# Optimization experiments

Measured on AMD Instinct MI355X. Metric: run time of the kernel, lower is better.

The kernel has to match this reference:

```python
import jax, jax.numpy as jnp
import numpy as np

MAX_NUM_CENTERS = 100
CENTER_IGNORE_PX = 3
SIGMA = 2.0   # center_gt_blur
KSIZE = 21    # GaussianLayer kernel size (ReflectionPad2d(10) + Conv2d(k=21))


def _gauss_kernel():
    r = KSIZE // 2
    x = jnp.arange(-r, r + 1, dtype=jnp.float32)
    g = jnp.exp(-0.5 * (x / SIGMA) ** 2)
    g = g / g.sum()
    return jnp.outer(g, g)  # [21,21], sums to 1 (matches scipy gaussian_filter of a delta)


def _gaussian_blur(x):
    # x: [B,H,W] -> depthwise 21x21 gaussian with reflect padding (GaussianLayer)
    r = KSIZE // 2
    k = _gauss_kernel()[None, None]  # [1,1,21,21]
    xp = jnp.pad(x[:, None], ((0, 0), (0, 0), (r, r), (r, r)), mode="reflect")
    y = jax.lax.conv_general_dilated(xp, k, (1, 1), "VALID",
                                     dimension_numbers=("NCHW", "OIHW", "NCHW"))
    return y[:, 0]


def setup_inputs() -> dict:
    key = jax.random.key(0)
    k1, k2 = jax.random.split(key)
    B, H, W = 8, 768, 768
    instances = jax.random.randint(k1, (B, 1, H, W), 0, MAX_NUM_CENTERS, dtype=jnp.int32)
    centers = jax.random.uniform(k2, (B, MAX_NUM_CENTERS, 2), dtype=jnp.float32) * (H - 1) + 1.0
    return {"instances": instances, "centers": centers}


def reference(instances, centers):
    B, _, H, W = instances.shape
    inst = instances[:, 0]                                # [B,H,W]
    col = jnp.arange(W, dtype=jnp.float32)                # xym_s[0][i,j] = j
    row = jnp.arange(H, dtype=jnp.float32)[:, None]       # xym_s[1][i,j] = i

    valid = inst > 0                                      # instance_mask
    has_inst = jnp.any(valid, axis=(1, 2)).astype(jnp.float32)  # len(unique)>1 gate

    # per-pixel nearest-center gather: center = centers[b, id-1]
    idx = jnp.clip(inst - 1, 0, MAX_NUM_CENTERS - 1)
    c = centers[jnp.arange(B)[:, None, None], idx]        # [B,H,W,2]
    gt_cx = jnp.where(valid, c[..., 1], -10000.0)         # gt_center_x (swapped coords)
    gt_cy = jnp.where(valid, c[..., 0], -10000.0)

    gt_X = gt_cx - row                                    # gt_center_x - xym_s[1]
    gt_Y = gt_cy - col                                    # gt_center_y - xym_s[0]

    near = (jnp.abs(gt_X) < CENTER_IGNORE_PX) & (jnp.abs(gt_Y) < CENTER_IGNORE_PX)
    # batches with no instances skip the block -> ignore stays all-ones
    ignore = jnp.where(has_inst[:, None, None] > 0, (~near).astype(jnp.float32), 1.0)

    m = valid.astype(jnp.float32)
    R = jnp.sqrt(gt_X ** 2 + gt_Y ** 2) * m
    theta_raw = jnp.arctan2(gt_Y, gt_X)
    theta = theta_raw * has_inst[:, None, None]           # skipped (zero) when no instances
    s = jnp.sin(theta_raw) * m
    cth = jnp.cos(theta_raw) * m
    M = jnp.sqrt(s ** 2 + cth ** 2)                       # == m, kept for faithfulness
    s = jnp.where(valid, s / jnp.maximum(M, 1e-12), 0.0)
    cth = jnp.where(valid, cth / jnp.maximum(M, 1e-12), 0.0)

    # gt_center_mask: zeros if no center-neighborhood pixels, else normalized blur
    blur = _gaussian_blur(1.0 - ignore)
    all_ones = jnp.all(ignore >= 1.0, axis=(1, 2))        # gt_center_mask.all()
    bmax = jnp.max(blur, axis=(1, 2), keepdims=True)
    cmask = jnp.where(all_ones[:, None, None], 0.0, blur / jnp.maximum(bmax, 1e-12))

    top = jnp.stack([R, theta, s, cth, ignore, cmask], axis=1)       # [B,6,H,W]
    mat = jnp.concatenate([top, jnp.zeros((B, 7, H, W), top.dtype)], axis=1)[:, :, None]
    # mat: [B,13,1,H,W]; channels 6..12 are zero (no orientation input)

    # gt_centers[id] = centers[b, id-1][[1,0]] for each instance id present
    present = jnp.zeros((B, MAX_NUM_CENTERS), dtype=bool).at[
        jnp.arange(B)[:, None], inst.reshape(B, -1)].set(True)
    swapped = centers[..., ::-1]
    gt_centers = jnp.zeros_like(centers).at[:, 1:, :].set(
        jnp.where(present[:, 1:, None], swapped[:, :-1, :], 0.0))

    return mat, gt_centers
```

## Files before the change

### kernel.cpp

```cpp
#include <hip/hip_runtime.h>
#include <math.h>

#define NB 8
#define NH 768
#define NW 768
#define NHW (NH*NW)
#define NCEN 100
#define NPIX (NB*NHW)
#define RAD 10
#define KS 21

#define SCAN_BLKS (NPIX / 4096)
#define BLKS_PER_B (NHW / 4096)
#define CAND_BLKS 96
#define ZBLKS 1344
#define ZPB 6144
#define ZBLK_PER_B 168
#define MID_BLKS (NB*CAND_BLKS + ZBLKS)
#define NPQ 3
#define FBLK_PX (NPQ*1024)
#define QBLK3_PER_B (NHW / FBLK_PX)
#define BSLOT 24
#define BCAP 23
#define GCAP 256
#define FCAP 256

#define STORE(v, p) (*(p) = (v))

#define OFF_MASKS 0
#define OFF_BLIST 4608
#define OFF_BMAXP 32256
#define OFF_HAS   33024
#define OFF_M     33032
#define OFF_GLIST 33040
#define WS_INTS   35088

typedef float f4 __attribute__((ext_vector_type(4)));

__device__ const float g_G[KS] = {
    7.4335e-7f, 7.9919e-6f, 6.6915e-5f, 0.00043634f, 0.00221592f,
    0.00876415f, 0.02699548f, 0.06475880f, 0.12098536f, 0.17603266f,
    0.19947114f,
    0.17603266f, 0.12098536f, 0.06475880f, 0.02699548f, 0.00876415f,
    0.00221592f, 0.00043634f, 6.6915e-5f, 7.9919e-6f, 7.4335e-7f};

__device__ __forceinline__ float wfun(int p, int q, const float* __restrict__ g) {
    int d = p - q;
    float w = 0.f;
    if (d >= -RAD && d <= RAD) w = g[d + RAD];
    int a = p + q;
    if (q > 0 && a <= RAD) w += g[a + RAD];
    if (q < NH - 1 && a >= 2 * (NH - 1) - RAD) w += g[a - 2 * (NH - 1) + RAD];
    return w;
}

__device__ __forceinline__ float fatan2(float Y, float X) {
    float ax = fabsf(X), ay = fabsf(Y);
    float mx = fmaxf(ax, ay), mn = fminf(ax, ay);
    float a = mx > 0.f ? __fdividef(mn, mx) : 0.f;
    float ss = a * a;
    float r = fmaf(fmaf(fmaf(fmaf(fmaf(-0.01172120f, ss, 0.05265332f), ss,
                -0.11643287f), ss, 0.19354346f), ss, -0.33262347f), ss, 0.99997726f) * a;
    if (ay > ax) r = 1.57079637f - r;
    if (X < 0.f) r = 3.14159274f - r;
    return copysignf(r, Y);
}

template <bool U8>
__global__ __launch_bounds__(256) void k_scan(const int4* __restrict__ inst4,
                                              const float* __restrict__ centers,
                                              int* __restrict__ ws,
                                              unsigned char* __restrict__ u8) {
    __shared__ unsigned sm[4];
    __shared__ float2 s_c2[NCEN];
    __shared__ int s_loc[BCAP];
    __shared__ int s_lcnt;
    __shared__ unsigned s_u8[1024];
    int t = threadIdx.x;
    int blk = blockIdx.x;
    int b = blk / BLKS_PER_B;
    int lblk = blk - b * BLKS_PER_B;
    if (t < 4) sm[t] = 0;
    if (t == 0) s_lcnt = 0;
    for (int k = t; k < NCEN; k += 256)
        s_c2[k] = ((const float2*)centers)[b * NCEN + k];
    __syncthreads();

    unsigned m0 = 0, m1 = 0, m2 = 0, m3 = 0;
    size_t base = (size_t)blk * 1024 + t;
    int ppb = lblk * 4096 + t * 4;
#pragma unroll
    for (int q = 0; q < 4; q++) {
        int4 v = inst4[base + (size_t)q * 256];
        int pp = ppb + q * 1024;
        int i = pp / NW;
        int j0 = pp - i * NW;
        if (U8) {
            unsigned packed = ((unsigned)v.x & 255u) | (((unsigned)v.y & 255u) << 8) |
                              (((unsigned)v.z & 255u) << 16) | (((unsigned)v.w & 255u) << 24);
            s_u8[q * 256 + t] = packed;
        }
        int a[4] = {v.x, v.y, v.z, v.w};
#pragma unroll
        for (int e = 0; e < 4; e++) {
            int iv = a[e];
            if (iv > 0) {
                unsigned bit = 1u << (iv & 31);
                int w = iv >> 5;
                if (w == 0) m0 |= bit; else if (w == 1) m1 |= bit;
                else if (w == 2) m2 |= bit; else m3 |= bit;
                int idx = iv - 1;
                idx = idx > NCEN - 1 ? NCEN - 1 : idx;
                float2 c = s_c2[idx];
                if (fabsf(c.y - (float)i) < 3.f && fabsf(c.x - (float)(j0 + e)) < 3.f) {
                    int slot = atomicAdd(&s_lcnt, 1);
                    if (slot < BCAP) s_loc[slot] = (i << 16) | (j0 + e);
                }
            }
        }
    }
#pragma unroll
    for (int off = 32; off >= 1; off >>= 1) {
        m0 |= __shfl_xor(m0, off);
        m1 |= __shfl_xor(m1, off);
        m2 |= __shfl_xor(m2, off);
        m3 |= __shfl_xor(m3, off);
    }
    if ((t & 63) == 0) {
        if (m0) atomicOr(&sm[0], m0);
        if (m1) atomicOr(&sm[1], m1);
        if (m2) atomicOr(&sm[2], m2);
        if (m3) atomicOr(&sm[3], m3);
    }
    __syncthreads();
    if (U8) {
        int4 vv = ((const int4*)s_u8)[t];
        *(int4*)&u8[(size_t)blk * 4096 + t * 16] = vv;
    }
    if (t < 4) ws[OFF_MASKS + blk * 4 + t] = (int)sm[t];
    int cnt = s_lcnt < BCAP ? s_lcnt : BCAP;
    int* slot = &ws[OFF_BLIST + blk * BSLOT];
    if (t == 0) slot[0] = cnt;
    if (t < cnt) slot[1 + t] = s_loc[t];
}

__global__ __launch_bounds__(256) void k_mid(const float* __restrict__ centers,
                                             int* __restrict__ ws,
                                             float* __restrict__ out) {
    int t = threadIdx.x;
    int g = blockIdx.x;

    if (g < NB * CAND_BLKS) {
        __shared__ float s_g[KS];
        __shared__ int s_list[GCAP];
        __shared__ int s_tot;
        __shared__ unsigned s_m[4];
        __shared__ float s_red[4];
        int b = g / CAND_BLKS;
        int cb = g - b * CAND_BLKS;
        if (t < KS) s_g[t] = g_G[t];
        if (t == 0) s_tot = 0;
        if (t < 4) s_m[t] = 0;
        __syncthreads();
        if (t < BLKS_PER_B) {
            const int* slot = &ws[OFF_BLIST + (b * BLKS_PER_B + t) * BSLOT];
            int cnt = slot[0];
            cnt = cnt < 0 ? 0 : (cnt > BCAP ? BCAP : cnt);
            int basep = atomicAdd(&s_tot, cnt);
            for (int i2 = 0; i2 < cnt; i2++) {
                int s = basep + i2;
                if (s < GCAP) s_list[s] = slot[1 + i2];
            }
            if (cb == 0) {
                const unsigned* pm = (const unsigned*)&ws[OFF_MASKS + (b * BLKS_PER_B + t) * 4];
                unsigned w0 = pm[0], w1 = pm[1], w2 = pm[2], w3 = pm[3];
                if (w0) atomicOr(&s_m[0], w0);
                if (w1) atomicOr(&s_m[1], w1);
                if (w2) atomicOr(&s_m[2], w2);
                if (w3) atomicOr(&s_m[3], w3);
            }
        }
        __syncthreads();
        int M = s_tot < GCAP ? s_tot : GCAP;

        if (cb == 0) {
            float* gt = out + (size_t)NB * 13 * NHW;
            if (t < NCEN) {
                float vx = 0.f, vy = 0.f;
                if (t >= 1 && ((s_m[t >> 5] >> (t & 31)) & 1u)) {
                    vx = centers[(b * NCEN + (t - 1)) * 2 + 1];
                    vy = centers[(b * NCEN + (t - 1)) * 2 + 0];
                }
                gt[(b * NCEN + t) * 2 + 0] = vx;
                gt[(b * NCEN + t) * 2 + 1] = vy;
            }
            if (t == 0) {
                unsigned any = (s_m[0] & 0xFFFFFFFEu) | s_m[1] | s_m[2] | s_m[3];
                ws[OFF_HAS + b] = any ? 1 : 0;
                ws[OFF_M + b] = M;
            }
            for (int e = t; e < M; e += 256) ws[OFF_GLIST + b * GCAP + e] = s_list[e];
        }

        float lmax = 0.f;
        int total = M * (KS * KS);
        for (int c = cb * 256 + t; c < total; c += CAND_BLKS * 256) {
            int m = c / (KS * KS), r = c - m * (KS * KS);
            int e = s_list[m];
            int pi = (e >> 16) + r / KS - RAD;
            int pj = (e & 0xFFFF) + (r - (r / KS) * KS) - RAD;
            if (pi < 0 || pi >= NH || pj < 0 || pj >= NW) continue;
            float acc = 0.f;
            for (int m2 = 0; m2 < M; m2++) {
                int e2 = s_list[m2];
                float wi = wfun(pi, e2 >> 16, s_g);
                if (wi == 0.f) continue;
                acc += wi * wfun(pj, e2 & 0xFFFF, s_g);
            }
            lmax = fmaxf(lmax, acc);
        }
#pragma unroll
        for (int off = 32; off >= 1; off >>= 1) lmax = fmaxf(lmax, __shfl_down(lmax, off));
        if ((t & 63) == 0) s_red[t >> 6] = lmax;
        __syncthreads();
        if (t == 0) {
            float bmx = fmaxf(fmaxf(s_red[0], s_red[1]), fmaxf(s_red[2], s_red[3]));
            ((float*)ws)[OFF_BMAXP + b * CAND_BLKS + cb] = bmx;
        }
    } else {
        int zblk = g - NB * CAND_BLKS;
        int b2 = zblk / ZBLK_PER_B;
        int rem0 = (zblk - b2 * ZBLK_PER_B) * ZPB;
        f4 z = {0.f, 0.f, 0.f, 0.f};
        f4* dst = (f4*)out + (size_t)b2 * (13 * NHW / 4) + (6 * NHW / 4) + rem0 + t;
#pragma unroll
        for (int it = 0; it < ZPB / 256; ++it)
            STORE(z, dst + it * 256);
    }
}

template <bool U8>
__global__ __launch_bounds__(256) void k_fused(const int* __restrict__ inst,
                                               const unsigned char* __restrict__ u8,
                                               const float* __restrict__ centers,
                                               const int* __restrict__ ws,
                                               float* __restrict__ out) {
    __shared__ float s_cen[2 * NCEN];
    __shared__ float s_g[KS];
    __shared__ int s_fl[FCAP];
    __shared__ int s_fM;
    __shared__ unsigned s_bm;
    int t = threadIdx.x;
    int b = blockIdx.x / QBLK3_PER_B;
    int qblk = blockIdx.x - b * QBLK3_PER_B;

    int has = ws[OFF_HAS + b];
    int M = ws[OFF_M + b];
    for (int k = t; k < 2 * NCEN; k += 256) s_cen[k] = centers[b * 2 * NCEN + k];
    if (t < KS) s_g[t] = g_G[t];
    if (t == 255) s_fM = 0;
    if (t == 254) s_bm = 0;
    __syncthreads();

    if (t < CAND_BLKS)
        atomicMax(&s_bm, __float_as_uint(((const float*)ws)[OFF_BMAXP + b * CAND_BLKS + t]));

    int p0blk = qblk * FBLK_PX;
    int r0 = qblk * 4;
    const int* gl = &ws[OFF_GLIST + b * GCAP];
    for (int m = t; m < M; m += 256) {
        int e = gl[m];
        int qi = e >> 16;
        bool keep = false;
#pragma unroll
        for (int rr = 0; rr < 4; rr++) keep |= (wfun(r0 + rr, qi, s_g) != 0.f);
        if (keep) {
            int slot = atomicAdd(&s_fM, 1);
            if (slot < FCAP) s_fl[slot] = e;
        }
    }
    __syncthreads();
    int FM = s_fM < FCAP ? s_fM : FCAP;
    float bmx = __uint_as_float(s_bm);
    float sc = (has && M > 0) ? 1.f / fmaxf(bmx, 1e-12f) : 0.f;

    float* outb = out + (size_t)b * 13 * NHW;

    for (int qq = 0; qq < NPQ; ++qq) {
        int p0 = p0blk + qq * 1024 + t * 4;
        int gi = p0 / NW;
        int gj0 = p0 - gi * NW;

        int ia[4];
        if (U8) {
            unsigned v8 = *(const unsigned*)&u8[(size_t)b * NHW + p0];
            ia[0] = v8 & 255; ia[1] = (v8 >> 8) & 255; ia[2] = (v8 >> 16) & 255; ia[3] = v8 >> 24;
        } else {
            int4 ivv = *(const int4*)&inst[(size_t)b * NHW + p0];
            ia[0] = ivv.x; ia[1] = ivv.y; ia[2] = ivv.z; ia[3] = ivv.w;
        }
        f4 vR, vTh, vS, vC, vIg;
#pragma unroll
        for (int e = 0; e < 4; e++) {
            int iv = ia[e];
            bool valid = iv > 0;
            int idx = iv - 1;
            idx = idx < 0 ? 0 : idx;
            float cy = s_cen[2 * idx];
            float cx = s_cen[2 * idx + 1];
            float gcx = valid ? cx : -10000.f;
            float gcy = valid ? cy : -10000.f;
            float X = gcx - (float)gi;
            float Y = gcy - (float)(gj0 + e);
            bool near = (fabsf(X) < 3.f) && (fabsf(Y) < 3.f);
            vIg[e] = (has != 0) ? (near ? 0.f : 1.f) : 1.f;
            float m = valid ? 1.f : 0.f;
            float R2 = X * X + Y * Y;
            vR[e] = sqrtf(R2) * m;
            float rinv = R2 > 0.f ? rsqrtf(R2) : 0.f;
            vS[e] = valid ? Y * rinv : 0.f;
            vC[e] = valid ? (R2 > 0.f ? X * rinv : 1.f) : 0.f;
            float th = fatan2(Y, X);
            vTh[e] = (has != 0) ? th : 0.f;
        }

        f4 blur = {0.f, 0.f, 0.f, 0.f};
        for (int m = 0; m < FM; m++) {
            int e2 = s_fl[m];
            float wi = wfun(gi, e2 >> 16, s_g);
            if (wi == 0.f) continue;
            int qj = e2 & 0xFFFF;
#pragma unroll
            for (int e = 0; e < 4; e++) blur[e] += wi * wfun(gj0 + e, qj, s_g);
        }
        f4 vCm = blur * sc;

        STORE(vR,  (f4*)&outb[(size_t)0 * NHW + p0]);
        STORE(vTh, (f4*)&outb[(size_t)1 * NHW + p0]);
        STORE(vS,  (f4*)&outb[(size_t)2 * NHW + p0]);
        STORE(vC,  (f4*)&outb[(size_t)3 * NHW + p0]);
        STORE(vIg, (f4*)&outb[(size_t)4 * NHW + p0]);
        STORE(vCm, (f4*)&outb[(size_t)5 * NHW + p0]);
    }
}

extern "C" void kernel_launch(void* const* d_in, const int* in_sizes, int n_in,
                              void* d_out, int out_size, void* d_ws, size_t ws_size,
                              hipStream_t stream) {
    const int* inst = (const int*)d_in[0];
    const float* centers = (const float*)d_in[1];
    float* out = (float*)d_out;
    int* ws = (int*)d_ws;
    unsigned char* u8 = (unsigned char*)d_ws + (size_t)WS_INTS * 4;
    bool use_u8 = ws_size >= (size_t)WS_INTS * 4 + (size_t)NPIX;

    if (use_u8) {
        k_scan<true><<<SCAN_BLKS, 256, 0, stream>>>((const int4*)inst, centers, ws, u8);
        k_mid<<<MID_BLKS, 256, 0, stream>>>(centers, ws, out);
        k_fused<true><<<NB * QBLK3_PER_B, 256, 0, stream>>>(inst, u8, centers, ws, out);
    } else {
        k_scan<false><<<SCAN_BLKS, 256, 0, stream>>>((const int4*)inst, centers, ws, u8);
        k_mid<<<MID_BLKS, 256, 0, stream>>>(centers, ws, out);
        k_fused<false><<<NB * QBLK3_PER_B, 256, 0, stream>>>(inst, u8, centers, ws, out);
    }
}
```

Measured before the change: 271.9 us.

## Compute per-pixel geometry channels and zero fill in the scan kernel

```diff
diff --git a/kernel.cpp b/kernel.cpp
--- a/kernel.cpp
+++ b/kernel.cpp
@@ -13,10 +13,6 @@
 #define SCAN_BLKS (NPIX / 4096)
 #define BLKS_PER_B (NHW / 4096)
 #define CAND_BLKS 96
-#define ZBLKS 1344
-#define ZPB 6144
-#define ZBLK_PER_B 168
-#define MID_BLKS (NB*CAND_BLKS + ZBLKS)
 #define NPQ 3
 #define FBLK_PX (NPQ*1024)
 #define QBLK3_PER_B (NHW / FBLK_PX)
@@ -33,7 +29,6 @@
 #define OFF_HAS   33024
 #define OFF_M     33032
 #define OFF_GLIST 33040
-#define WS_INTS   35088
 
 typedef float f4 __attribute__((ext_vector_type(4)));
 
@@ -66,16 +61,14 @@
     return copysignf(r, Y);
 }
 
-template <bool U8>
-__global__ __launch_bounds__(256) void k_scan(const int4* __restrict__ inst4,
+__global__ __launch_bounds__(256) void k_main(const int4* __restrict__ inst4,
                                               const float* __restrict__ centers,
                                               int* __restrict__ ws,
-                                              unsigned char* __restrict__ u8) {
+                                              float* __restrict__ out) {
     __shared__ unsigned sm[4];
     __shared__ float2 s_c2[NCEN];
     __shared__ int s_loc[BCAP];
     __shared__ int s_lcnt;
-    __shared__ unsigned s_u8[1024];
     int t = threadIdx.x;
     int blk = blockIdx.x;
     int b = blk / BLKS_PER_B;
@@ -89,35 +82,55 @@
     unsigned m0 = 0, m1 = 0, m2 = 0, m3 = 0;
     size_t base = (size_t)blk * 1024 + t;
     int ppb = lblk * 4096 + t * 4;
+    float* outb = out + (size_t)b * 13 * NHW;
+    const f4 z = {0.f, 0.f, 0.f, 0.f};
 #pragma unroll
     for (int q = 0; q < 4; q++) {
         int4 v = inst4[base + (size_t)q * 256];
         int pp = ppb + q * 1024;
-        int i = pp / NW;
-        int j0 = pp - i * NW;
-        if (U8) {
-            unsigned packed = ((unsigned)v.x & 255u) | (((unsigned)v.y & 255u) << 8) |
-                              (((unsigned)v.z & 255u) << 16) | (((unsigned)v.w & 255u) << 24);
-            s_u8[q * 256 + t] = packed;
-        }
-        int a[4] = {v.x, v.y, v.z, v.w};
+        int gi = pp / NW;
+        int gj0 = pp - gi * NW;
+        int ia[4] = {v.x, v.y, v.z, v.w};
+        f4 vR, vTh, vS, vC, vIg;
 #pragma unroll
         for (int e = 0; e < 4; e++) {
-            int iv = a[e];
-            if (iv > 0) {
+            int iv = ia[e];
+            bool valid = iv > 0;
+            if (valid) {
                 unsigned bit = 1u << (iv & 31);
                 int w = iv >> 5;
                 if (w == 0) m0 |= bit; else if (w == 1) m1 |= bit;
                 else if (w == 2) m2 |= bit; else m3 |= bit;
-                int idx = iv - 1;
-                idx = idx > NCEN - 1 ? NCEN - 1 : idx;
-                float2 c = s_c2[idx];
-                if (fabsf(c.y - (float)i) < 3.f && fabsf(c.x - (float)(j0 + e)) < 3.f) {
-                    int slot = atomicAdd(&s_lcnt, 1);
-                    if (slot < BCAP) s_loc[slot] = (i << 16) | (j0 + e);
-                }
             }
-        }
+            int idx = iv - 1;
+            idx = idx < 0 ? 0 : (idx > NCEN - 1 ? NCEN - 1 : idx);
+            float2 c = s_c2[idx];
+            float gcx = valid ? c.y : -10000.f;
+            float gcy = valid ? c.x : -10000.f;
+            float X = gcx - (float)gi;
+            float Y = gcy - (float)(gj0 + e);
+            bool near = (fabsf(X) < 3.f) && (fabsf(Y) < 3.f);
+            if (valid && near) {
+                int slot = atomicAdd(&s_lcnt, 1);
+                if (slot < BCAP) s_loc[slot] = (gi << 16) | (gj0 + e);
+            }
+            vIg[e] = near ? 0.f : 1.f;
+            float m = valid ? 1.f : 0.f;
+            float R2 = X * X + Y * Y;
+            vR[e] = sqrtf(R2) * m;
+            float rinv = R2 > 0.f ? rsqrtf(R2) : 0.f;
+            vS[e] = valid ? Y * rinv : 0.f;
+            vC[e] = valid ? (R2 > 0.f ? X * rinv : 1.f) : 0.f;
+            vTh[e] = fatan2(Y, X);
+        }
+        STORE(vR,  (f4*)&outb[(size_t)0 * NHW + pp]);
+        STORE(vTh, (f4*)&outb[(size_t)1 * NHW + pp]);
+        STORE(vS,  (f4*)&outb[(size_t)2 * NHW + pp]);
+        STORE(vC,  (f4*)&outb[(size_t)3 * NHW + pp]);
+        STORE(vIg, (f4*)&outb[(size_t)4 * NHW + pp]);
+#pragma unroll
+        for (int ch = 6; ch < 13; ++ch)
+            STORE(z, (f4*)&outb[(size_t)ch * NHW + pp]);
     }
 #pragma unroll
     for (int off = 32; off >= 1; off >>= 1) {
@@ -133,10 +146,6 @@
         if (m3) atomicOr(&sm[3], m3);
     }
     __syncthreads();
-    if (U8) {
-        int4 vv = ((const int4*)s_u8)[t];
-        *(int4*)&u8[(size_t)blk * 4096 + t * 16] = vv;
-    }
     if (t < 4) ws[OFF_MASKS + blk * 4 + t] = (int)sm[t];
     int cnt = s_lcnt < BCAP ? s_lcnt : BCAP;
     int* slot = &ws[OFF_BLIST + blk * BSLOT];
@@ -144,108 +153,90 @@
     if (t < cnt) slot[1 + t] = s_loc[t];
 }
 
-__global__ __launch_bounds__(256) void k_mid(const float* __restrict__ centers,
-                                             int* __restrict__ ws,
-                                             float* __restrict__ out) {
+__global__ __launch_bounds__(256) void k_bmax(const float* __restrict__ centers,
+                                              int* __restrict__ ws,
+                                              float* __restrict__ out) {
+    __shared__ float s_g[KS];
+    __shared__ int s_list[GCAP];
+    __shared__ int s_tot;
+    __shared__ unsigned s_m[4];
+    __shared__ float s_red[4];
     int t = threadIdx.x;
-    int g = blockIdx.x;
-
-    if (g < NB * CAND_BLKS) {
-        __shared__ float s_g[KS];
-        __shared__ int s_list[GCAP];
-        __shared__ int s_tot;
-        __shared__ unsigned s_m[4];
-        __shared__ float s_red[4];
-        int b = g / CAND_BLKS;
-        int cb = g - b * CAND_BLKS;
-        if (t < KS) s_g[t] = g_G[t];
-        if (t == 0) s_tot = 0;
-        if (t < 4) s_m[t] = 0;
-        __syncthreads();
-        if (t < BLKS_PER_B) {
-            const int* slot = &ws[OFF_BLIST + (b * BLKS_PER_B + t) * BSLOT];
-            int cnt = slot[0];
-            cnt = cnt < 0 ? 0 : (cnt > BCAP ? BCAP : cnt);
-            int basep = atomicAdd(&s_tot, cnt);
-            for (int i2 = 0; i2 < cnt; i2++) {
-                int s = basep + i2;
-                if (s < GCAP) s_list[s] = slot[1 + i2];
+    int b = blockIdx.x / CAND_BLKS;
+    int cb = blockIdx.x - b * CAND_BLKS;
+    if (t < KS) s_g[t] = g_G[t];
+    if (t == 0) s_tot = 0;
+    if (t < 4) s_m[t] = 0;
+    __syncthreads();
+    if (t < BLKS_PER_B) {
+        const int* slot = &ws[OFF_BLIST + (b * BLKS_PER_B + t) * BSLOT];
+        int cnt = slot[0];
+        cnt = cnt < 0 ? 0 : (cnt > BCAP ? BCAP : cnt);
+        int basep = atomicAdd(&s_tot, cnt);
+        for (int i2 = 0; i2 < cnt; i2++) {
+            int s = basep + i2;
+            if (s < GCAP) s_list[s] = slot[1 + i2];
+        }
+        if (cb == 0) {
+            const unsigned* pm = (const unsigned*)&ws[OFF_MASKS + (b * BLKS_PER_B + t) * 4];
+            unsigned w0 = pm[0], w1 = pm[1], w2 = pm[2], w3 = pm[3];
+            if (w0) atomicOr(&s_m[0], w0);
+            if (w1) atomicOr(&s_m[1], w1);
+            if (w2) atomicOr(&s_m[2], w2);
+            if (w3) atomicOr(&s_m[3], w3);
+        }
+    }
+    __syncthreads();
+    int M = s_tot < GCAP ? s_tot : GCAP;
+
+    if (cb == 0) {
+        float* gt = out + (size_t)NB * 13 * NHW;
+        if (t < NCEN) {
+            float vx = 0.f, vy = 0.f;
+            if (t >= 1 && ((s_m[t >> 5] >> (t & 31)) & 1u)) {
+                vx = centers[(b * NCEN + (t - 1)) * 2 + 1];
+                vy = centers[(b * NCEN + (t - 1)) * 2 + 0];
             }
-            if (cb == 0) {
-                const unsigned* pm = (const unsigned*)&ws[OFF_MASKS + (b * BLKS_PER_B + t) * 4];
-                unsigned w0 = pm[0], w1 = pm[1], w2 = pm[2], w3 = pm[3];
-                if (w0) atomicOr(&s_m[0], w0);
-                if (w1) atomicOr(&s_m[1], w1);
-                if (w2) atomicOr(&s_m[2], w2);
-                if (w3) atomicOr(&s_m[3], w3);
-            }
-        }
-        __syncthreads();
-        int M = s_tot < GCAP ? s_tot : GCAP;
-
-        if (cb == 0) {
-            float* gt = out + (size_t)NB * 13 * NHW;
-            if (t < NCEN) {
-                float vx = 0.f, vy = 0.f;
-                if (t >= 1 && ((s_m[t >> 5] >> (t & 31)) & 1u)) {
-                    vx = centers[(b * NCEN + (t - 1)) * 2 + 1];
-                    vy = centers[(b * NCEN + (t - 1)) * 2 + 0];
-                }
-                gt[(b * NCEN + t) * 2 + 0] = vx;
-                gt[(b * NCEN + t) * 2 + 1] = vy;
-            }
-            if (t == 0) {
-                unsigned any = (s_m[0] & 0xFFFFFFFEu) | s_m[1] | s_m[2] | s_m[3];
-                ws[OFF_HAS + b] = any ? 1 : 0;
-                ws[OFF_M + b] = M;
-            }
-            for (int e = t; e < M; e += 256) ws[OFF_GLIST + b * GCAP + e] = s_list[e];
-        }
-
-        float lmax = 0.f;
-        int total = M * (KS * KS);
-        for (int c = cb * 256 + t; c < total; c += CAND_BLKS * 256) {
-            int m = c / (KS * KS), r = c - m * (KS * KS);
-            int e = s_list[m];
-            int pi = (e >> 16) + r / KS - RAD;
-            int pj = (e & 0xFFFF) + (r - (r / KS) * KS) - RAD;
-            if (pi < 0 || pi >= NH || pj < 0 || pj >= NW) continue;
-            float acc = 0.f;
-            for (int m2 = 0; m2 < M; m2++) {
-                int e2 = s_list[m2];
-                float wi = wfun(pi, e2 >> 16, s_g);
-                if (wi == 0.f) continue;
-                acc += wi * wfun(pj, e2 & 0xFFFF, s_g);
-            }
-            lmax = fmaxf(lmax, acc);
-        }
-#pragma unroll
-        for (int off = 32; off >= 1; off >>= 1) lmax = fmaxf(lmax, __shfl_down(lmax, off));
-        if ((t & 63) == 0) s_red[t >> 6] = lmax;
-        __syncthreads();
+            gt[(b * NCEN + t) * 2 + 0] = vx;
+            gt[(b * NCEN + t) * 2 + 1] = vy;
+        }
         if (t == 0) {
-            float bmx = fmaxf(fmaxf(s_red[0], s_red[1]), fmaxf(s_red[2], s_red[3]));
-            ((float*)ws)[OFF_BMAXP + b * CAND_BLKS + cb] = bmx;
-        }
-    } else {
-        int zblk = g - NB * CAND_BLKS;
-        int b2 = zblk / ZBLK_PER_B;
-        int rem0 = (zblk - b2 * ZBLK_PER_B) * ZPB;
-        f4 z = {0.f, 0.f, 0.f, 0.f};
-        f4* dst = (f4*)out + (size_t)b2 * (13 * NHW / 4) + (6 * NHW / 4) + rem0 + t;
-#pragma unroll
-        for (int it = 0; it < ZPB / 256; ++it)
-            STORE(z, dst + it * 256);
-    }
-}
-
-template <bool U8>
-__global__ __launch_bounds__(256) void k_fused(const int* __restrict__ inst,
-                                               const unsigned char* __restrict__ u8,
-                                               const float* __restrict__ centers,
-                                               const int* __restrict__ ws,
+            unsigned any = (s_m[0] & 0xFFFFFFFEu) | s_m[1] | s_m[2] | s_m[3];
+            ws[OFF_HAS + b] = any ? 1 : 0;
+            ws[OFF_M + b] = M;
+        }
+        for (int e = t; e < M; e += 256) ws[OFF_GLIST + b * GCAP + e] = s_list[e];
+    }
+
+    float lmax = 0.f;
+    int total = M * (KS * KS);
+    for (int c = cb * 256 + t; c < total; c += CAND_BLKS * 256) {
+        int m = c / (KS * KS), r = c - m * (KS * KS);
+        int e = s_list[m];
+        int pi = (e >> 16) + r / KS - RAD;
+        int pj = (e & 0xFFFF) + (r - (r / KS) * KS) - RAD;
+        if (pi < 0 || pi >= NH || pj < 0 || pj >= NW) continue;
+        float acc = 0.f;
+        for (int m2 = 0; m2 < M; m2++) {
+            int e2 = s_list[m2];
+            float wi = wfun(pi, e2 >> 16, s_g);
+            if (wi == 0.f) continue;
+            acc += wi * wfun(pj, e2 & 0xFFFF, s_g);
+        }
+        lmax = fmaxf(lmax, acc);
+    }
+#pragma unroll
+    for (int off = 32; off >= 1; off >>= 1) lmax = fmaxf(lmax, __shfl_down(lmax, off));
+    if ((t & 63) == 0) s_red[t >> 6] = lmax;
+    __syncthreads();
+    if (t == 0) {
+        float bmx = fmaxf(fmaxf(s_red[0], s_red[1]), fmaxf(s_red[2], s_red[3]));
+        ((float*)ws)[OFF_BMAXP + b * CAND_BLKS + cb] = bmx;
+    }
+}
+
+__global__ __launch_bounds__(256) void k_cmask(const int* __restrict__ ws,
                                                float* __restrict__ out) {
-    __shared__ float s_cen[2 * NCEN];
     __shared__ float s_g[KS];
     __shared__ int s_fl[FCAP];
     __shared__ int s_fM;
@@ -256,7 +247,6 @@
 
     int has = ws[OFF_HAS + b];
     int M = ws[OFF_M + b];
-    for (int k = t; k < 2 * NCEN; k += 256) s_cen[k] = centers[b * 2 * NCEN + k];
     if (t < KS) s_g[t] = g_G[t];
     if (t == 255) s_fM = 0;
     if (t == 254) s_bm = 0;
@@ -285,45 +275,11 @@
     float sc = (has && M > 0) ? 1.f / fmaxf(bmx, 1e-12f) : 0.f;
 
     float* outb = out + (size_t)b * 13 * NHW;
-
+    const f4 z = {0.f, 0.f, 0.f, 0.f};
     for (int qq = 0; qq < NPQ; ++qq) {
         int p0 = p0blk + qq * 1024 + t * 4;
         int gi = p0 / NW;
         int gj0 = p0 - gi * NW;
-
-        int ia[4];
-        if (U8) {
-            unsigned v8 = *(const unsigned*)&u8[(size_t)b * NHW + p0];
-            ia[0] = v8 & 255; ia[1] = (v8 >> 8) & 255; ia[2] = (v8 >> 16) & 255; ia[3] = v8 >> 24;
-        } else {
-            int4 ivv = *(const int4*)&inst[(size_t)b * NHW + p0];
-            ia[0] = ivv.x; ia[1] = ivv.y; ia[2] = ivv.z; ia[3] = ivv.w;
-        }
-        f4 vR, vTh, vS, vC, vIg;
-#pragma unroll
-        for (int e = 0; e < 4; e++) {
-            int iv = ia[e];
-            bool valid = iv > 0;
-            int idx = iv - 1;
-            idx = idx < 0 ? 0 : idx;
-            float cy = s_cen[2 * idx];
-            float cx = s_cen[2 * idx + 1];
-            float gcx = valid ? cx : -10000.f;
-            float gcy = valid ? cy : -10000.f;
-            float X = gcx - (float)gi;
-            float Y = gcy - (float)(gj0 + e);
-            bool near = (fabsf(X) < 3.f) && (fabsf(Y) < 3.f);
-            vIg[e] = (has != 0) ? (near ? 0.f : 1.f) : 1.f;
-            float m = valid ? 1.f : 0.f;
-            float R2 = X * X + Y * Y;
-            vR[e] = sqrtf(R2) * m;
-            float rinv = R2 > 0.f ? rsqrtf(R2) : 0.f;
-            vS[e] = valid ? Y * rinv : 0.f;
-            vC[e] = valid ? (R2 > 0.f ? X * rinv : 1.f) : 0.f;
-            float th = fatan2(Y, X);
-            vTh[e] = (has != 0) ? th : 0.f;
-        }
-
         f4 blur = {0.f, 0.f, 0.f, 0.f};
         for (int m = 0; m < FM; m++) {
             int e2 = s_fl[m];
@@ -334,13 +290,9 @@
             for (int e = 0; e < 4; e++) blur[e] += wi * wfun(gj0 + e, qj, s_g);
         }
         f4 vCm = blur * sc;
-
-        STORE(vR,  (f4*)&outb[(size_t)0 * NHW + p0]);
-        STORE(vTh, (f4*)&outb[(size_t)1 * NHW + p0]);
-        STORE(vS,  (f4*)&outb[(size_t)2 * NHW + p0]);
-        STORE(vC,  (f4*)&outb[(size_t)3 * NHW + p0]);
-        STORE(vIg, (f4*)&outb[(size_t)4 * NHW + p0]);
         STORE(vCm, (f4*)&outb[(size_t)5 * NHW + p0]);
+        if (!has)
+            STORE(z, (f4*)&outb[(size_t)1 * NHW + p0]);
     }
 }
 
@@ -351,16 +303,8 @@
     const float* centers = (const float*)d_in[1];
     float* out = (float*)d_out;
     int* ws = (int*)d_ws;
-    unsigned char* u8 = (unsigned char*)d_ws + (size_t)WS_INTS * 4;
-    bool use_u8 = ws_size >= (size_t)WS_INTS * 4 + (size_t)NPIX;
-
-    if (use_u8) {
-        k_scan<true><<<SCAN_BLKS, 256, 0, stream>>>((const int4*)inst, centers, ws, u8);
-        k_mid<<<MID_BLKS, 256, 0, stream>>>(centers, ws, out);
-        k_fused<true><<<NB * QBLK3_PER_B, 256, 0, stream>>>(inst, u8, centers, ws, out);
-    } else {
-        k_scan<false><<<SCAN_BLKS, 256, 0, stream>>>((const int4*)inst, centers, ws, u8);
-        k_mid<<<MID_BLKS, 256, 0, stream>>>(centers, ws, out);
-        k_fused<false><<<NB * QBLK3_PER_B, 256, 0, stream>>>(inst, u8, centers, ws, out);
-    }
-}
+
+    k_main<<<SCAN_BLKS, 256, 0, stream>>>((const int4*)inst, centers, ws, out);
+    k_bmax<<<NB * CAND_BLKS, 256, 0, stream>>>(centers, ws, out);
+    k_cmask<<<NB * QBLK3_PER_B, 256, 0, stream>>>(ws, out);
+}
```

After: 294.7 us. 8.4% more time.

## Split output work per channel plane and move zero-fill into the output kernel

Applied to the files above, without the earlier changes.

```diff
diff --git a/kernel.cpp b/kernel.cpp
--- a/kernel.cpp
+++ b/kernel.cpp
@@ -13,17 +13,13 @@
 #define SCAN_BLKS (NPIX / 4096)
 #define BLKS_PER_B (NHW / 4096)
 #define CAND_BLKS 96
-#define ZBLKS 1344
-#define ZPB 6144
-#define ZBLK_PER_B 168
-#define MID_BLKS (NB*CAND_BLKS + ZBLKS)
-#define NPQ 3
-#define FBLK_PX (NPQ*1024)
-#define QBLK3_PER_B (NHW / FBLK_PX)
+#define CHUNKS 24
+#define CHUNK_F4 6144
+#define OUT_BLKS (NB*13*CHUNKS)
 #define BSLOT 24
 #define BCAP 23
 #define GCAP 256
-#define FCAP 256
+#define FCAP 96
 
 #define STORE(v, p) (*(p) = (v))
 
@@ -144,203 +140,202 @@
     if (t < cnt) slot[1 + t] = s_loc[t];
 }
 
-__global__ __launch_bounds__(256) void k_mid(const float* __restrict__ centers,
-                                             int* __restrict__ ws,
+__global__ __launch_bounds__(256) void k_bmax(const float* __restrict__ centers,
+                                              int* __restrict__ ws,
+                                              float* __restrict__ out) {
+    __shared__ float s_g[KS];
+    __shared__ int s_list[GCAP];
+    __shared__ int s_tot;
+    __shared__ unsigned s_m[4];
+    __shared__ float s_red[4];
+    int t = threadIdx.x;
+    int b = blockIdx.x / CAND_BLKS;
+    int cb = blockIdx.x - b * CAND_BLKS;
+    if (t < KS) s_g[t] = g_G[t];
+    if (t == 0) s_tot = 0;
+    if (t < 4) s_m[t] = 0;
+    __syncthreads();
+    if (t < BLKS_PER_B) {
+        const int* slot = &ws[OFF_BLIST + (b * BLKS_PER_B + t) * BSLOT];
+        int cnt = slot[0];
+        cnt = cnt < 0 ? 0 : (cnt > BCAP ? BCAP : cnt);
+        int basep = atomicAdd(&s_tot, cnt);
+        for (int i2 = 0; i2 < cnt; i2++) {
+            int s = basep + i2;
+            if (s < GCAP) s_list[s] = slot[1 + i2];
+        }
+        if (cb == 0) {
+            const unsigned* pm = (const unsigned*)&ws[OFF_MASKS + (b * BLKS_PER_B + t) * 4];
+            unsigned w0 = pm[0], w1 = pm[1], w2 = pm[2], w3 = pm[3];
+            if (w0) atomicOr(&s_m[0], w0);
+            if (w1) atomicOr(&s_m[1], w1);
+            if (w2) atomicOr(&s_m[2], w2);
+            if (w3) atomicOr(&s_m[3], w3);
+        }
+    }
+    __syncthreads();
+    int M = s_tot < GCAP ? s_tot : GCAP;
+
+    if (cb == 0) {
+        float* gt = out + (size_t)NB * 13 * NHW;
+        if (t < NCEN) {
+            float vx = 0.f, vy = 0.f;
+            if (t >= 1 && ((s_m[t >> 5] >> (t & 31)) & 1u)) {
+                vx = centers[(b * NCEN + (t - 1)) * 2 + 1];
+                vy = centers[(b * NCEN + (t - 1)) * 2 + 0];
+            }
+            gt[(b * NCEN + t) * 2 + 0] = vx;
+            gt[(b * NCEN + t) * 2 + 1] = vy;
+        }
+        if (t == 0) {
+            unsigned any = (s_m[0] & 0xFFFFFFFEu) | s_m[1] | s_m[2] | s_m[3];
+            ws[OFF_HAS + b] = any ? 1 : 0;
+            ws[OFF_M + b] = M;
+        }
+        for (int e = t; e < M; e += 256) ws[OFF_GLIST + b * GCAP + e] = s_list[e];
+    }
+
+    float lmax = 0.f;
+    int total = M * (KS * KS);
+    for (int c = cb * 256 + t; c < total; c += CAND_BLKS * 256) {
+        int m = c / (KS * KS), r = c - m * (KS * KS);
+        int e = s_list[m];
+        int pi = (e >> 16) + r / KS - RAD;
+        int pj = (e & 0xFFFF) + (r - (r / KS) * KS) - RAD;
+        if (pi < 0 || pi >= NH || pj < 0 || pj >= NW) continue;
+        float acc = 0.f;
+        for (int m2 = 0; m2 < M; m2++) {
+            int e2 = s_list[m2];
+            float wi = wfun(pi, e2 >> 16, s_g);
+            if (wi == 0.f) continue;
+            acc += wi * wfun(pj, e2 & 0xFFFF, s_g);
+        }
+        lmax = fmaxf(lmax, acc);
+    }
+#pragma unroll
+    for (int off = 32; off >= 1; off >>= 1) lmax = fmaxf(lmax, __shfl_down(lmax, off));
+    if ((t & 63) == 0) s_red[t >> 6] = lmax;
+    __syncthreads();
+    if (t == 0) {
+        float bmx = fmaxf(fmaxf(s_red[0], s_red[1]), fmaxf(s_red[2], s_red[3]));
+        ((float*)ws)[OFF_BMAXP + b * CAND_BLKS + cb] = bmx;
+    }
+}
+
+template <bool U8>
+__global__ __launch_bounds__(256) void k_out(const int* __restrict__ inst,
+                                             const unsigned char* __restrict__ u8,
+                                             const float* __restrict__ centers,
+                                             const int* __restrict__ ws,
                                              float* __restrict__ out) {
     int t = threadIdx.x;
-    int g = blockIdx.x;
-
-    if (g < NB * CAND_BLKS) {
+    int blk = blockIdx.x;
+    int plane = blk / CHUNKS;
+    int chunk = blk - plane * CHUNKS;
+    int b = plane / 13;
+    int ch = plane - b * 13;
+    f4* dst = (f4*)(out + (size_t)b * 13 * NHW + (size_t)ch * NHW) + chunk * CHUNK_F4;
+
+    if (ch >= 6) {
+        const f4 z = {0.f, 0.f, 0.f, 0.f};
+#pragma unroll
+        for (int it = 0; it < CHUNK_F4 / 256; ++it) STORE(z, dst + it * 256 + t);
+        return;
+    }
+
+    if (ch == 5) {
         __shared__ float s_g[KS];
-        __shared__ int s_list[GCAP];
-        __shared__ int s_tot;
-        __shared__ unsigned s_m[4];
-        __shared__ float s_red[4];
-        int b = g / CAND_BLKS;
-        int cb = g - b * CAND_BLKS;
+        __shared__ int s_fl[FCAP];
+        __shared__ int s_fM;
+        __shared__ unsigned s_bm;
+        int has = ws[OFF_HAS + b];
+        int M = ws[OFF_M + b];
         if (t < KS) s_g[t] = g_G[t];
-        if (t == 0) s_tot = 0;
-        if (t < 4) s_m[t] = 0;
+        if (t == 255) s_fM = 0;
+        if (t == 254) s_bm = 0;
         __syncthreads();
-        if (t < BLKS_PER_B) {
-            const int* slot = &ws[OFF_BLIST + (b * BLKS_PER_B + t) * BSLOT];
-            int cnt = slot[0];
-            cnt = cnt < 0 ? 0 : (cnt > BCAP ? BCAP : cnt);
-            int basep = atomicAdd(&s_tot, cnt);
-            for (int i2 = 0; i2 < cnt; i2++) {
-                int s = basep + i2;
-                if (s < GCAP) s_list[s] = slot[1 + i2];
-            }
-            if (cb == 0) {
-                const unsigned* pm = (const unsigned*)&ws[OFF_MASKS + (b * BLKS_PER_B + t) * 4];
-                unsigned w0 = pm[0], w1 = pm[1], w2 = pm[2], w3 = pm[3];
-                if (w0) atomicOr(&s_m[0], w0);
-                if (w1) atomicOr(&s_m[1], w1);
-                if (w2) atomicOr(&s_m[2], w2);
-                if (w3) atomicOr(&s_m[3], w3);
+        if (t < CAND_BLKS)
+            atomicMax(&s_bm, __float_as_uint(((const float*)ws)[OFF_BMAXP + b * CAND_BLKS + t]));
+        int r0 = chunk * 32;
+        const int* gl = &ws[OFF_GLIST + b * GCAP];
+        for (int m = t; m < M; m += 256) {
+            int e = gl[m];
+            int qi = e >> 16;
+            if (qi >= r0 - RAD && qi < r0 + 32 + RAD) {
+                int slot = atomicAdd(&s_fM, 1);
+                if (slot < FCAP) s_fl[slot] = e;
             }
         }
         __syncthreads();
-        int M = s_tot < GCAP ? s_tot : GCAP;
-
-        if (cb == 0) {
-            float* gt = out + (size_t)NB * 13 * NHW;
-            if (t < NCEN) {
-                float vx = 0.f, vy = 0.f;
-                if (t >= 1 && ((s_m[t >> 5] >> (t & 31)) & 1u)) {
-                    vx = centers[(b * NCEN + (t - 1)) * 2 + 1];
-                    vy = centers[(b * NCEN + (t - 1)) * 2 + 0];
-                }
-                gt[(b * NCEN + t) * 2 + 0] = vx;
-                gt[(b * NCEN + t) * 2 + 1] = vy;
-            }
-            if (t == 0) {
-                unsigned any = (s_m[0] & 0xFFFFFFFEu) | s_m[1] | s_m[2] | s_m[3];
-                ws[OFF_HAS + b] = any ? 1 : 0;
-                ws[OFF_M + b] = M;
-            }
-            for (int e = t; e < M; e += 256) ws[OFF_GLIST + b * GCAP + e] = s_list[e];
-        }
-
-        float lmax = 0.f;
-        int total = M * (KS * KS);
-        for (int c = cb * 256 + t; c < total; c += CAND_BLKS * 256) {
-            int m = c / (KS * KS), r = c - m * (KS * KS);
-            int e = s_list[m];
-            int pi = (e >> 16) + r / KS - RAD;
-            int pj = (e & 0xFFFF) + (r - (r / KS) * KS) - RAD;
-            if (pi < 0 || pi >= NH || pj < 0 || pj >= NW) continue;
-            float acc = 0.f;
-            for (int m2 = 0; m2 < M; m2++) {
-                int e2 = s_list[m2];
-                float wi = wfun(pi, e2 >> 16, s_g);
+        int FM = s_fM < FCAP ? s_fM : FCAP;
+        float sc = (has && M > 0) ? 1.f / fmaxf(__uint_as_float(s_bm), 1e-12f) : 0.f;
+        for (int it = 0; it < CHUNK_F4 / 256; ++it) {
+            int f = chunk * CHUNK_F4 + it * 256 + t;
+            int p0 = f * 4;
+            int gi = p0 / NW, gj0 = p0 - gi * NW;
+            f4 blur = {0.f, 0.f, 0.f, 0.f};
+            for (int m = 0; m < FM; m++) {
+                int e2 = s_fl[m];
+                float wi = wfun(gi, e2 >> 16, s_g);
                 if (wi == 0.f) continue;
-                acc += wi * wfun(pj, e2 & 0xFFFF, s_g);
-            }
-            lmax = fmaxf(lmax, acc);
-        }
-#pragma unroll
-        for (int off = 32; off >= 1; off >>= 1) lmax = fmaxf(lmax, __shfl_down(lmax, off));
-        if ((t & 63) == 0) s_red[t >> 6] = lmax;
-        __syncthreads();
-        if (t == 0) {
-            float bmx = fmaxf(fmaxf(s_red[0], s_red[1]), fmaxf(s_red[2], s_red[3]));
-            ((float*)ws)[OFF_BMAXP + b * CAND_BLKS + cb] = bmx;
-        }
-    } else {
-        int zblk = g - NB * CAND_BLKS;
-        int b2 = zblk / ZBLK_PER_B;
-        int rem0 = (zblk - b2 * ZBLK_PER_B) * ZPB;
-        f4 z = {0.f, 0.f, 0.f, 0.f};
-        f4* dst = (f4*)out + (size_t)b2 * (13 * NHW / 4) + (6 * NHW / 4) + rem0 + t;
-#pragma unroll
-        for (int it = 0; it < ZPB / 256; ++it)
-            STORE(z, dst + it * 256);
-    }
-}
-
-template <bool U8>
-__global__ __launch_bounds__(256) void k_fused(const int* __restrict__ inst,
-                                               const unsigned char* __restrict__ u8,
-                                               const float* __restrict__ centers,
-                                               const int* __restrict__ ws,
-                                               float* __restrict__ out) {
-    __shared__ float s_cen[2 * NCEN];
-    __shared__ float s_g[KS];
-    __shared__ int s_fl[FCAP];
-    __shared__ int s_fM;
-    __shared__ unsigned s_bm;
-    int t = threadIdx.x;
-    int b = blockIdx.x / QBLK3_PER_B;
-    int qblk = blockIdx.x - b * QBLK3_PER_B;
-
+                int qj = e2 & 0xFFFF;
+#pragma unroll
+                for (int e = 0; e < 4; e++) blur[e] += wi * wfun(gj0 + e, qj, s_g);
+            }
+            f4 v = blur * sc;
+            STORE(v, dst + it * 256 + t);
+        }
+        return;
+    }
+
+    __shared__ float2 s_c2[NCEN];
+    for (int k = t; k < NCEN; k += 256)
+        s_c2[k] = ((const float2*)centers)[b * NCEN + k];
     int has = ws[OFF_HAS + b];
-    int M = ws[OFF_M + b];
-    for (int k = t; k < 2 * NCEN; k += 256) s_cen[k] = centers[b * 2 * NCEN + k];
-    if (t < KS) s_g[t] = g_G[t];
-    if (t == 255) s_fM = 0;
-    if (t == 254) s_bm = 0;
-    __syncthreads();
-
-    if (t < CAND_BLKS)
-        atomicMax(&s_bm, __float_as_uint(((const float*)ws)[OFF_BMAXP + b * CAND_BLKS + t]));
-
-    int p0blk = qblk * FBLK_PX;
-    int r0 = qblk * 4;
-    const int* gl = &ws[OFF_GLIST + b * GCAP];
-    for (int m = t; m < M; m += 256) {
-        int e = gl[m];
-        int qi = e >> 16;
-        bool keep = false;
-#pragma unroll
-        for (int rr = 0; rr < 4; rr++) keep |= (wfun(r0 + rr, qi, s_g) != 0.f);
-        if (keep) {
-            int slot = atomicAdd(&s_fM, 1);
-            if (slot < FCAP) s_fl[slot] = e;
-        }
-    }
-    __syncthreads();
-    int FM = s_fM < FCAP ? s_fM : FCAP;
-    float bmx = __uint_as_float(s_bm);
-    float sc = (has && M > 0) ? 1.f / fmaxf(bmx, 1e-12f) : 0.f;
-
-    float* outb = out + (size_t)b * 13 * NHW;
-
-    for (int qq = 0; qq < NPQ; ++qq) {
-        int p0 = p0blk + qq * 1024 + t * 4;
-        int gi = p0 / NW;
-        int gj0 = p0 - gi * NW;
-
+    __syncthreads();
+    for (int it = 0; it < CHUNK_F4 / 256; ++it) {
+        int f = chunk * CHUNK_F4 + it * 256 + t;
+        int p0 = f * 4;
+        int gi = p0 / NW, gj0 = p0 - gi * NW;
         int ia[4];
         if (U8) {
             unsigned v8 = *(const unsigned*)&u8[(size_t)b * NHW + p0];
-            ia[0] = v8 & 255; ia[1] = (v8 >> 8) & 255; ia[2] = (v8 >> 16) & 255; ia[3] = v8 >> 24;
+            ia[0] = v8 & 255; ia[1] = (v8 >> 8) & 255;
+            ia[2] = (v8 >> 16) & 255; ia[3] = v8 >> 24;
         } else {
             int4 ivv = *(const int4*)&inst[(size_t)b * NHW + p0];
             ia[0] = ivv.x; ia[1] = ivv.y; ia[2] = ivv.z; ia[3] = ivv.w;
         }
-        f4 vR, vTh, vS, vC, vIg;
+        f4 o;
 #pragma unroll
         for (int e = 0; e < 4; e++) {
             int iv = ia[e];
             bool valid = iv > 0;
             int idx = iv - 1;
             idx = idx < 0 ? 0 : idx;
-            float cy = s_cen[2 * idx];
-            float cx = s_cen[2 * idx + 1];
-            float gcx = valid ? cx : -10000.f;
-            float gcy = valid ? cy : -10000.f;
+            float2 c = s_c2[idx];
+            float gcx = valid ? c.y : -10000.f;
+            float gcy = valid ? c.x : -10000.f;
             float X = gcx - (float)gi;
             float Y = gcy - (float)(gj0 + e);
-            bool near = (fabsf(X) < 3.f) && (fabsf(Y) < 3.f);
-            vIg[e] = (has != 0) ? (near ? 0.f : 1.f) : 1.f;
-            float m = valid ? 1.f : 0.f;
-            float R2 = X * X + Y * Y;
-            vR[e] = sqrtf(R2) * m;
-            float rinv = R2 > 0.f ? rsqrtf(R2) : 0.f;
-            vS[e] = valid ? Y * rinv : 0.f;
-            vC[e] = valid ? (R2 > 0.f ? X * rinv : 1.f) : 0.f;
-            float th = fatan2(Y, X);
-            vTh[e] = (has != 0) ? th : 0.f;
-        }
-
-        f4 blur = {0.f, 0.f, 0.f, 0.f};
-        for (int m = 0; m < FM; m++) {
-            int e2 = s_fl[m];
-            float wi = wfun(gi, e2 >> 16, s_g);
-            if (wi == 0.f) continue;
-            int qj = e2 & 0xFFFF;
-#pragma unroll
-            for (int e = 0; e < 4; e++) blur[e] += wi * wfun(gj0 + e, qj, s_g);
-        }
-        f4 vCm = blur * sc;
-
-        STORE(vR,  (f4*)&outb[(size_t)0 * NHW + p0]);
-        STORE(vTh, (f4*)&outb[(size_t)1 * NHW + p0]);
-        STORE(vS,  (f4*)&outb[(size_t)2 * NHW + p0]);
-        STORE(vC,  (f4*)&outb[(size_t)3 * NHW + p0]);
-        STORE(vIg, (f4*)&outb[(size_t)4 * NHW + p0]);
-        STORE(vCm, (f4*)&outb[(size_t)5 * NHW + p0]);
+            if (ch == 0) {
+                o[e] = sqrtf(X * X + Y * Y) * (valid ? 1.f : 0.f);
+            } else if (ch == 1) {
+                o[e] = has ? fatan2(Y, X) : 0.f;
+            } else if (ch == 2) {
+                float R2 = X * X + Y * Y;
+                float rinv = R2 > 0.f ? rsqrtf(R2) : 0.f;
+                o[e] = valid ? Y * rinv : 0.f;
+            } else if (ch == 3) {
+                float R2 = X * X + Y * Y;
+                float rinv = R2 > 0.f ? rsqrtf(R2) : 0.f;
+                o[e] = valid ? (R2 > 0.f ? X * rinv : 1.f) : 0.f;
+            } else {
+                bool near = (fabsf(X) < 3.f) && (fabsf(Y) < 3.f);
+                o[e] = near ? 0.f : 1.f;
+            }
+        }
+        STORE(o, dst + it * 256 + t);
     }
 }
 
@@ -356,11 +351,11 @@
 
     if (use_u8) {
         k_scan<true><<<SCAN_BLKS, 256, 0, stream>>>((const int4*)inst, centers, ws, u8);
-        k_mid<<<MID_BLKS, 256, 0, stream>>>(centers, ws, out);
-        k_fused<true><<<NB * QBLK3_PER_B, 256, 0, stream>>>(inst, u8, centers, ws, out);
+        k_bmax<<<NB * CAND_BLKS, 256, 0, stream>>>(centers, ws, out);
+        k_out<true><<<OUT_BLKS, 256, 0, stream>>>(inst, u8, centers, ws, out);
     } else {
         k_scan<false><<<SCAN_BLKS, 256, 0, stream>>>((const int4*)inst, centers, ws, u8);
-        k_mid<<<MID_BLKS, 256, 0, stream>>>(centers, ws, out);
-        k_fused<false><<<NB * QBLK3_PER_B, 256, 0, stream>>>(inst, u8, centers, ws, out);
-    }
-}
+        k_bmax<<<NB * CAND_BLKS, 256, 0, stream>>>(centers, ws, out);
+        k_out<false><<<OUT_BLKS, 256, 0, stream>>>(inst, u8, centers, ws, out);
+    }
+}
```

After: 306.6 us. 1.13x slower.
